# Performance work log

Hardware: AMD Instinct MI355X
Metric: run time of the kernel (lower is better)

Reference implementation:

```python
import jax, jax.numpy as jnp
import numpy as np

HEADS = 8
D = 1024


def setup_inputs() -> dict:
    key = jax.random.key(0)
    ks = jax.random.split(key, 10)
    B, Sq, Sk = 8, 2048, 2048
    x = jax.random.normal(ks[0], (B, Sq, D), dtype=jnp.float32)
    context = jax.random.normal(ks[1], (B, Sk, D), dtype=jnp.float32)
    # Dense params (glorot-ish scale)
    def dense(k, fin, fout):
        return jax.random.normal(k, (fin, fout), dtype=jnp.float32) / np.sqrt(fin)
    Wq = dense(ks[2], D, HEADS); bq = jnp.zeros((HEADS,), jnp.float32)
    Wk = dense(ks[3], D, HEADS); bk = jnp.zeros((HEADS,), jnp.float32)
    Wv = dense(ks[4], D, HEADS); bv = jnp.zeros((HEADS,), jnp.float32)
    Wo = dense(ks[5], HEADS, D); bo = jnp.zeros((D,), jnp.float32)
    return {"x": x, "context": context, "Wq": Wq, "bq": bq,
            "Wk": Wk, "bk": bk, "Wv": Wv, "bv": bv, "Wo": Wo, "bo": bo}


def reference(x, context, Wq, bq, Wk, bk, Wv, bv, Wo, bo):
    # q: [B,Sq,H], k/v: [B,Sk,H]  (H = heads = projection width, no head split)
    q = jnp.einsum('bsd,dh->bsh', x, Wq) + bq
    k = jnp.einsum('btd,dh->bth', context, Wk) + bk
    v = jnp.einsum('btd,dh->bth', context, Wv) + bv
    # Dot(axes=-1): scores[b,s,t] = q[b,s,:] . k[b,t,:]  -> [B,Sq,Sk]
    scores = jnp.einsum('bsh,bth->bst', q, k)
    weights = jax.nn.softmax(scores, axis=-1)  # no 1/sqrt(d) scaling in original
    # Dot(axes=(-1,1)): out[b,s,h] = sum_t weights[b,s,t] * v[b,t,h]
    out = jnp.einsum('bst,bth->bsh', weights, v)
    return jnp.einsum('bsh,hd->bsd', out, Wo) + bo
```

## Files before the change

### kernel.cpp

```cpp
#include <hip/hip_runtime.h>

constexpr int D = 1024;
constexpr int H = 8;
constexpr int S = 2048;
constexpr int B = 8;
constexpr int NROW = B * S;

__global__ __launch_bounds__(512)
void proj_kernel(const float* __restrict__ x, const float* __restrict__ ctx,
                 const float* __restrict__ Wq, const float* __restrict__ bq,
                 const float* __restrict__ Wk, const float* __restrict__ bk,
                 const float* __restrict__ Wv, const float* __restrict__ bv,
                 float* __restrict__ qo, float* __restrict__ ko,
                 float* __restrict__ vo)
{
    __shared__ float part[8][64][17];
    const int tid  = threadIdx.x;
    const int lane = tid & 63;
    const int wid  = __builtin_amdgcn_readfirstlane(tid >> 6);
    const bool kv  = (int)blockIdx.x >= (NROW / 64);
    const int blk  = kv ? ((int)blockIdx.x - NROW / 64) : (int)blockIdx.x;
    const int row  = blk * 64 + lane;

    const float4* s4 = (const float4*)((kv ? ctx : x) + (size_t)row * D);
    const int kf0 = wid * 32;

    float acc[16];
#pragma unroll
    for (int c = 0; c < 16; ++c) acc[c] = 0.f;

    if (!kv) {
#pragma unroll 4
        for (int j = 0; j < 32; ++j) {
            const float4 xr = s4[kf0 + j];
            const int k0 = (kf0 + j) * 4;
#pragma unroll
            for (int e = 0; e < 4; ++e) {
                const float xs = (&xr.x)[e];
                const float* wr = Wq + (size_t)(k0 + e) * 8;
#pragma unroll
                for (int h = 0; h < 8; ++h) acc[h] += xs * wr[h];
            }
        }
    } else {
#pragma unroll 2
        for (int j = 0; j < 32; ++j) {
            const float4 xr = s4[kf0 + j];
            const int k0 = (kf0 + j) * 4;
#pragma unroll
            for (int e = 0; e < 4; ++e) {
                const float xs = (&xr.x)[e];
                const float* wkr = Wk + (size_t)(k0 + e) * 8;
                const float* wvr = Wv + (size_t)(k0 + e) * 8;
#pragma unroll
                for (int h = 0; h < 8; ++h) {
                    acc[h]     += xs * wkr[h];
                    acc[8 + h] += xs * wvr[h];
                }
            }
        }
    }

#pragma unroll
    for (int c = 0; c < 16; ++c) part[wid][lane][c] = acc[c];
    __syncthreads();

    const int r = tid >> 3, h = tid & 7;
    const int orow = blk * 64 + r;
    if (!kv) {
        float s0 = 0.f;
#pragma unroll
        for (int w = 0; w < 8; ++w) s0 += part[w][r][h];
        qo[(size_t)orow * H + h] = s0 + bq[h];
    } else {
        float s0 = 0.f, s1 = 0.f;
#pragma unroll
        for (int w = 0; w < 8; ++w) { s0 += part[w][r][h]; s1 += part[w][r][h + 8]; }
        ko[(size_t)orow * H + h] = s0 + bk[h];
        vo[(size_t)orow * H + h] = s1 + bv[h];
    }
}

constexpr int ROWS_PER_WAVE = 4;
constexpr int ROWS_PER_BLOCK = 16;
constexpr int TILE_T = 512;

__global__ __launch_bounds__(256)
void attn_kernel(const float* __restrict__ q, const float* __restrict__ k,
                 const float* __restrict__ v, const float* __restrict__ Wo,
                 const float* __restrict__ bo, float* __restrict__ out)
{
    __shared__ float4 kt[TILE_T * 2];
    __shared__ float4 vt[TILE_T * 2];
    const int tid  = threadIdx.x;
    const int lane = tid & 63;
    const int wid  = tid >> 6;

    const int row0 = blockIdx.x * ROWS_PER_BLOCK + wid * ROWS_PER_WAVE;
    const int b = row0 >> 11;

    float qv[ROWS_PER_WAVE][H];
#pragma unroll
    for (int r = 0; r < ROWS_PER_WAVE; ++r) {
        const float4* q4 = (const float4*)(q + (size_t)(row0 + r) * H);
        const float4 a = q4[0], c = q4[1];
        qv[r][0] = a.x; qv[r][1] = a.y; qv[r][2] = a.z; qv[r][3] = a.w;
        qv[r][4] = c.x; qv[r][5] = c.y; qv[r][6] = c.z; qv[r][7] = c.w;
    }

    float l[ROWS_PER_WAVE] = {0.f, 0.f, 0.f, 0.f};
    float o[ROWS_PER_WAVE][H];
#pragma unroll
    for (int r = 0; r < ROWS_PER_WAVE; ++r)
#pragma unroll
        for (int h = 0; h < H; ++h) o[r][h] = 0.f;

    const float4* kg = (const float4*)(k + (size_t)b * S * H);
    const float4* vg = (const float4*)(v + (size_t)b * S * H);

    for (int tile = 0; tile < S / TILE_T; ++tile) {
        __syncthreads();
#pragma unroll
        for (int i = 0; i < 4; ++i) {
            kt[i * 256 + tid] = kg[tile * 1024 + i * 256 + tid];
            vt[i * 256 + tid] = vg[tile * 1024 + i * 256 + tid];
        }
        __syncthreads();
#pragma unroll 2
        for (int m = 0; m < TILE_T / 64; ++m) {
            const int t2 = (lane + (m << 6)) * 2;
            const float4 ka = kt[t2], kb = kt[t2 + 1];
            const float4 va = vt[t2], vb = vt[t2 + 1];
#pragma unroll
            for (int r = 0; r < ROWS_PER_WAVE; ++r) {
                const float s = qv[r][0] * ka.x + qv[r][1] * ka.y
                              + qv[r][2] * ka.z + qv[r][3] * ka.w
                              + qv[r][4] * kb.x + qv[r][5] * kb.y
                              + qv[r][6] * kb.z + qv[r][7] * kb.w;
                const float e = __expf(s);
                l[r] += e;
                o[r][0] += e * va.x; o[r][1] += e * va.y;
                o[r][2] += e * va.z; o[r][3] += e * va.w;
                o[r][4] += e * vb.x; o[r][5] += e * vb.y;
                o[r][6] += e * vb.z; o[r][7] += e * vb.w;
            }
        }
    }

#pragma unroll
    for (int r = 0; r < ROWS_PER_WAVE; ++r) {
#pragma unroll
        for (int off = 32; off > 0; off >>= 1) l[r] += __shfl_xor(l[r], off);
        const float inv = 1.f / l[r];
#pragma unroll
        for (int h = 0; h < H; ++h) {
#pragma unroll
            for (int off = 32; off > 0; off >>= 1) o[r][h] += __shfl_xor(o[r][h], off);
            o[r][h] *= inv;
        }
    }

    const float4* Wo4 = (const float4*)Wo;
    const float4* bo4 = (const float4*)bo;
    float4* out4 = (float4*)out;
#pragma unroll
    for (int c = 0; c < 4; ++c) {
        const int f = lane + 64 * c;
        float4 w[H];
#pragma unroll
        for (int h = 0; h < H; ++h) w[h] = Wo4[h * (D / 4) + f];
        const float4 base = bo4[f];
#pragma unroll
        for (int r = 0; r < ROWS_PER_WAVE; ++r) {
            float4 acc = base;
#pragma unroll
            for (int h = 0; h < H; ++h) {
                acc.x += o[r][h] * w[h].x;
                acc.y += o[r][h] * w[h].y;
                acc.z += o[r][h] * w[h].z;
                acc.w += o[r][h] * w[h].w;
            }
            out4[(size_t)(row0 + r) * (D / 4) + f] = acc;
        }
    }
}

extern "C" void kernel_launch(void* const* d_in, const int* in_sizes, int n_in,
                              void* d_out, int out_size, void* d_ws, size_t ws_size,
                              hipStream_t stream) {
    const float* x   = (const float*)d_in[0];
    const float* ctx = (const float*)d_in[1];
    const float* Wq  = (const float*)d_in[2];
    const float* bq  = (const float*)d_in[3];
    const float* Wk  = (const float*)d_in[4];
    const float* bk  = (const float*)d_in[5];
    const float* Wv  = (const float*)d_in[6];
    const float* bv  = (const float*)d_in[7];
    const float* Wo  = (const float*)d_in[8];
    const float* bo  = (const float*)d_in[9];
    float* out = (float*)d_out;

    float* qw = (float*)d_ws;
    float* kw = qw + (size_t)NROW * H;
    float* vw = kw + (size_t)NROW * H;

    proj_kernel<<<dim3(2 * NROW / 64), dim3(512), 0, stream>>>(
        x, ctx, Wq, bq, Wk, bk, Wv, bv, qw, kw, vw);
    attn_kernel<<<dim3(NROW / ROWS_PER_BLOCK), dim3(256), 0, stream>>>(
        qw, kw, vw, Wo, bo, out);
}
```

Before: 236.7 us.

## Stage projection weights in swizzled LDS and use 16-lane teams per row pair

The projection kernel now copies Wq (or Wk and Wv) into shared memory with an XOR swizzle, instead of reading the weights from global memory or scalar loads inside the inner loop. Each 16-thread team handles two rows, with lanes striding across the feature dimension so global loads are coalesced. Partial sums are reduced with shuffles rather than through a shared-memory partial array and a second sync. The cost is a larger LDS footprint (64KB for K/V blocks), which may reduce occupancy, plus per-block weight staging overhead.

```diff
diff --git a/kernel.cpp b/kernel.cpp
--- a/kernel.cpp
+++ b/kernel.cpp
@@ -5,6 +5,8 @@
 constexpr int S = 2048;
 constexpr int B = 8;
 constexpr int NROW = B * S;
+
+__device__ __forceinline__ int swz(int i) { return i ^ ((i >> 3) & 7); }
 
 __global__ __launch_bounds__(512)
 void proj_kernel(const float* __restrict__ x, const float* __restrict__ ctx,
@@ -14,70 +16,105 @@
                  float* __restrict__ qo, float* __restrict__ ko,
                  float* __restrict__ vo)
 {
-    __shared__ float part[8][64][17];
-    const int tid  = threadIdx.x;
-    const int lane = tid & 63;
-    const int wid  = __builtin_amdgcn_readfirstlane(tid >> 6);
-    const bool kv  = (int)blockIdx.x >= (NROW / 64);
-    const int blk  = kv ? ((int)blockIdx.x - NROW / 64) : (int)blockIdx.x;
-    const int row  = blk * 64 + lane;
-
-    const float4* s4 = (const float4*)((kv ? ctx : x) + (size_t)row * D);
-    const int kf0 = wid * 32;
-
-    float acc[16];
-#pragma unroll
-    for (int c = 0; c < 16; ++c) acc[c] = 0.f;
-
-    if (!kv) {
+    __shared__ float4 wlds[4096];
+    const int tid = threadIdx.x;
+    const bool kvb = (int)blockIdx.x >= (NROW / 64);
+    const int blk  = kvb ? ((int)blockIdx.x - NROW / 64) : (int)blockIdx.x;
+
+    if (!kvb) {
+        const float4* w4 = (const float4*)Wq;
+        for (int i = tid; i < 2048; i += 512) wlds[swz(i)] = w4[i];
+    } else {
+        const float4* a4 = (const float4*)Wk;
+        const float4* b4 = (const float4*)Wv;
+        for (int i = tid; i < 2048; i += 512) {
+            wlds[swz(i)]        = a4[i];
+            wlds[2048 + swz(i)] = b4[i];
+        }
+    }
+    __syncthreads();
+
+    const int c    = tid & 15;
+    const int team = tid >> 4;
+    const int row0 = blk * 64 + team * 2;
+    const float* src = kvb ? ctx : x;
+    const float4* r0 = (const float4*)(src + (size_t)row0 * D);
+    const float4* r1 = (const float4*)(src + (size_t)(row0 + 1) * D);
+
+    if (!kvb) {
+        float a0[8], a1[8];
+#pragma unroll
+        for (int h = 0; h < 8; ++h) { a0[h] = 0.f; a1[h] = 0.f; }
 #pragma unroll 4
-        for (int j = 0; j < 32; ++j) {
-            const float4 xr = s4[kf0 + j];
-            const int k0 = (kf0 + j) * 4;
+        for (int j = 0; j < 16; ++j) {
+            const float4 xa = r0[16 * j + c];
+            const float4 xb = r1[16 * j + c];
+            const int ib = 128 * j + 8 * c;
 #pragma unroll
             for (int e = 0; e < 4; ++e) {
-                const float xs = (&xr.x)[e];
-                const float* wr = Wq + (size_t)(k0 + e) * 8;
-#pragma unroll
-                for (int h = 0; h < 8; ++h) acc[h] += xs * wr[h];
+                const float4 w0 = wlds[swz(ib + 2 * e)];
+                const float4 w1 = wlds[swz(ib + 2 * e + 1)];
+                const float s0 = (&xa.x)[e], s1 = (&xb.x)[e];
+                a0[0] += s0 * w0.x; a0[1] += s0 * w0.y; a0[2] += s0 * w0.z; a0[3] += s0 * w0.w;
+                a0[4] += s0 * w1.x; a0[5] += s0 * w1.y; a0[6] += s0 * w1.z; a0[7] += s0 * w1.w;
+                a1[0] += s1 * w0.x; a1[1] += s1 * w0.y; a1[2] += s1 * w0.z; a1[3] += s1 * w0.w;
+                a1[4] += s1 * w1.x; a1[5] += s1 * w1.y; a1[6] += s1 * w1.z; a1[7] += s1 * w1.w;
+            }
+        }
+#pragma unroll
+        for (int h = 0; h < 8; ++h) {
+            float s0 = a0[h], s1 = a1[h];
+            s0 += __shfl_down(s0, 8); s1 += __shfl_down(s1, 8);
+            s0 += __shfl_down(s0, 4); s1 += __shfl_down(s1, 4);
+            s0 += __shfl_down(s0, 2); s1 += __shfl_down(s1, 2);
+            s0 += __shfl_down(s0, 1); s1 += __shfl_down(s1, 1);
+            if (c == 0) {
+                qo[(size_t)row0 * H + h]       = s0 + bq[h];
+                qo[(size_t)(row0 + 1) * H + h] = s1 + bq[h];
             }
         }
     } else {
+        float a0[16], a1[16];
+#pragma unroll
+        for (int h = 0; h < 16; ++h) { a0[h] = 0.f; a1[h] = 0.f; }
 #pragma unroll 2
-        for (int j = 0; j < 32; ++j) {
-            const float4 xr = s4[kf0 + j];
-            const int k0 = (kf0 + j) * 4;
+        for (int j = 0; j < 16; ++j) {
+            const float4 xa = r0[16 * j + c];
+            const float4 xb = r1[16 * j + c];
+            const int ib = 128 * j + 8 * c;
 #pragma unroll
             for (int e = 0; e < 4; ++e) {
-                const float xs = (&xr.x)[e];
-                const float* wkr = Wk + (size_t)(k0 + e) * 8;
-                const float* wvr = Wv + (size_t)(k0 + e) * 8;
-#pragma unroll
-                for (int h = 0; h < 8; ++h) {
-                    acc[h]     += xs * wkr[h];
-                    acc[8 + h] += xs * wvr[h];
+                const int i0 = swz(ib + 2 * e), i1 = swz(ib + 2 * e + 1);
+                const float4 k0 = wlds[i0],        k1 = wlds[i1];
+                const float4 v0 = wlds[2048 + i0], v1 = wlds[2048 + i1];
+                const float s0 = (&xa.x)[e], s1 = (&xb.x)[e];
+                a0[0]  += s0 * k0.x; a0[1]  += s0 * k0.y; a0[2]  += s0 * k0.z; a0[3]  += s0 * k0.w;
+                a0[4]  += s0 * k1.x; a0[5]  += s0 * k1.y; a0[6]  += s0 * k1.z; a0[7]  += s0 * k1.w;
+                a0[8]  += s0 * v0.x; a0[9]  += s0 * v0.y; a0[10] += s0 * v0.z; a0[11] += s0 * v0.w;
+                a0[12] += s0 * v1.x; a0[13] += s0 * v1.y; a0[14] += s0 * v1.z; a0[15] += s0 * v1.w;
+                a1[0]  += s1 * k0.x; a1[1]  += s1 * k0.y; a1[2]  += s1 * k0.z; a1[3]  += s1 * k0.w;
+                a1[4]  += s1 * k1.x; a1[5]  += s1 * k1.y; a1[6]  += s1 * k1.z; a1[7]  += s1 * k1.w;
+                a1[8]  += s1 * v0.x; a1[9]  += s1 * v0.y; a1[10] += s1 * v0.z; a1[11] += s1 * v0.w;
+                a1[12] += s1 * v1.x; a1[13] += s1 * v1.y; a1[14] += s1 * v1.z; a1[15] += s1 * v1.w;
+            }
+        }
+#pragma unroll
+        for (int h = 0; h < 16; ++h) {
+            float s0 = a0[h], s1 = a1[h];
+            s0 += __shfl_down(s0, 8); s1 += __shfl_down(s1, 8);
+            s0 += __shfl_down(s0, 4); s1 += __shfl_down(s1, 4);
+            s0 += __shfl_down(s0, 2); s1 += __shfl_down(s1, 2);
+            s0 += __shfl_down(s0, 1); s1 += __shfl_down(s1, 1);
+            if (c == 0) {
+                if (h < 8) {
+                    ko[(size_t)row0 * H + h]       = s0 + bk[h];
+                    ko[(size_t)(row0 + 1) * H + h] = s1 + bk[h];
+                } else {
+                    vo[(size_t)row0 * H + (h - 8)]       = s0 + bv[h - 8];
+                    vo[(size_t)(row0 + 1) * H + (h - 8)] = s1 + bv[h - 8];
                 }
             }
         }
-    }
-
-#pragma unroll
-    for (int c = 0; c < 16; ++c) part[wid][lane][c] = acc[c];
-    __syncthreads();
-
-    const int r = tid >> 3, h = tid & 7;
-    const int orow = blk * 64 + r;
-    if (!kv) {
-        float s0 = 0.f;
-#pragma unroll
-        for (int w = 0; w < 8; ++w) s0 += part[w][r][h];
-        qo[(size_t)orow * H + h] = s0 + bq[h];
-    } else {
-        float s0 = 0.f, s1 = 0.f;
-#pragma unroll
-        for (int w = 0; w < 8; ++w) { s0 += part[w][r][h]; s1 += part[w][r][h + 8]; }
-        ko[(size_t)orow * H + h] = s0 + bk[h];
-        vo[(size_t)orow * H + h] = s1 + bv[h];
     }
 }
 
```

New measurement: 230.9 us. 1.03x faster.

## Stage projection weights in LDS and split K/V projections into separate blocks

Applied to the files above, without the earlier changes.

The projection kernel now loads the full 1024x8 weight matrix for its projection into shared memory, then computes one projection per block using 256 threads with four K-slices per row. K and V get separate blocks instead of one fused block, giving more, lighter blocks with 8 accumulators each. Weight reads come from LDS rather than per-lane global loads, and register pressure drops. The trade-off is that the context tensor is now read twice from global memory, once for K and once for V, and each block must first copy the weights into LDS.

```diff
diff --git a/kernel.cpp b/kernel.cpp
--- a/kernel.cpp
+++ b/kernel.cpp
@@ -6,7 +6,7 @@
 constexpr int B = 8;
 constexpr int NROW = B * S;
 
-__global__ __launch_bounds__(512)
+__global__ __launch_bounds__(256)
 void proj_kernel(const float* __restrict__ x, const float* __restrict__ ctx,
                  const float* __restrict__ Wq, const float* __restrict__ bq,
                  const float* __restrict__ Wk, const float* __restrict__ bk,
@@ -14,70 +14,59 @@
                  float* __restrict__ qo, float* __restrict__ ko,
                  float* __restrict__ vo)
 {
-    __shared__ float part[8][64][17];
-    const int tid  = threadIdx.x;
-    const int lane = tid & 63;
-    const int wid  = __builtin_amdgcn_readfirstlane(tid >> 6);
-    const bool kv  = (int)blockIdx.x >= (NROW / 64);
-    const int blk  = kv ? ((int)blockIdx.x - NROW / 64) : (int)blockIdx.x;
-    const int row  = blk * 64 + lane;
-
-    const float4* s4 = (const float4*)((kv ? ctx : x) + (size_t)row * D);
-    const int kf0 = wid * 32;
-
-    float acc[16];
-#pragma unroll
-    for (int c = 0; c < 16; ++c) acc[c] = 0.f;
-
-    if (!kv) {
-#pragma unroll 4
-        for (int j = 0; j < 32; ++j) {
-            const float4 xr = s4[kf0 + j];
-            const int k0 = (kf0 + j) * 4;
-#pragma unroll
-            for (int e = 0; e < 4; ++e) {
-                const float xs = (&xr.x)[e];
-                const float* wr = Wq + (size_t)(k0 + e) * 8;
-#pragma unroll
-                for (int h = 0; h < 8; ++h) acc[h] += xs * wr[h];
-            }
-        }
-    } else {
-#pragma unroll 2
-        for (int j = 0; j < 32; ++j) {
-            const float4 xr = s4[kf0 + j];
-            const int k0 = (kf0 + j) * 4;
-#pragma unroll
-            for (int e = 0; e < 4; ++e) {
-                const float xs = (&xr.x)[e];
-                const float* wkr = Wk + (size_t)(k0 + e) * 8;
-                const float* wvr = Wv + (size_t)(k0 + e) * 8;
-#pragma unroll
-                for (int h = 0; h < 8; ++h) {
-                    acc[h]     += xs * wkr[h];
-                    acc[8 + h] += xs * wvr[h];
-                }
-            }
-        }
-    }
-
-#pragma unroll
-    for (int c = 0; c < 16; ++c) part[wid][lane][c] = acc[c];
+    __shared__ float4 wlds[2048];
+    __shared__ float  part[4 * 64 * 9];
+
+    const int bid = blockIdx.x;
+    int type, blk;
+    if (bid < NROW / 64) { type = 0; blk = bid; }
+    else { const int sub = bid - NROW / 64; blk = sub >> 1; type = 1 + (sub & 1); }
+
+    const float* W   = (type == 0) ? Wq : (type == 1) ? Wk : Wv;
+    const float* bb  = (type == 0) ? bq : (type == 1) ? bk : bv;
+    const float* src = (type == 0) ? x  : ctx;
+    float* dst       = (type == 0) ? qo : (type == 1) ? ko : vo;
+
+    const int tid = threadIdx.x, lane = tid & 63, w = tid >> 6;
+
+    const float4* W4 = (const float4*)W;
+    for (int i = tid; i < 2048; i += 256) wlds[i] = W4[i];
     __syncthreads();
 
-    const int r = tid >> 3, h = tid & 7;
-    const int orow = blk * 64 + r;
-    if (!kv) {
-        float s0 = 0.f;
-#pragma unroll
-        for (int w = 0; w < 8; ++w) s0 += part[w][r][h];
-        qo[(size_t)orow * H + h] = s0 + bq[h];
-    } else {
-        float s0 = 0.f, s1 = 0.f;
-#pragma unroll
-        for (int w = 0; w < 8; ++w) { s0 += part[w][r][h]; s1 += part[w][r][h + 8]; }
-        ko[(size_t)orow * H + h] = s0 + bk[h];
-        vo[(size_t)orow * H + h] = s1 + bv[h];
+    const int row = blk * 64 + lane;
+    const float4* r4 = (const float4*)(src + (size_t)row * D) + (w << 6);
+
+    float acc[8];
+#pragma unroll
+    for (int h = 0; h < 8; ++h) acc[h] = 0.f;
+
+#pragma unroll 8
+    for (int j = 0; j < 64; ++j) {
+        const float4 xv = r4[j];
+        const int kb = (w << 9) + (j << 3);
+#pragma unroll
+        for (int e = 0; e < 4; ++e) {
+            const float4 w0 = wlds[kb + 2 * e];
+            const float4 w1 = wlds[kb + 2 * e + 1];
+            const float xs = (&xv.x)[e];
+            acc[0] += xs * w0.x; acc[1] += xs * w0.y;
+            acc[2] += xs * w0.z; acc[3] += xs * w0.w;
+            acc[4] += xs * w1.x; acc[5] += xs * w1.y;
+            acc[6] += xs * w1.z; acc[7] += xs * w1.w;
+        }
+    }
+
+    const int pb = tid * 9;
+#pragma unroll
+    for (int h = 0; h < 8; ++h) part[pb + h] = acc[h];
+    __syncthreads();
+
+#pragma unroll
+    for (int idx = tid; idx < 512; idx += 256) {
+        const int r = idx >> 3, h = idx & 7;
+        const float s = part[r * 9 + h] + part[(64 + r) * 9 + h]
+                      + part[(128 + r) * 9 + h] + part[(192 + r) * 9 + h];
+        dst[(size_t)(blk * 64 + r) * H + h] = s + bb[h];
     }
 }
 
@@ -204,7 +193,7 @@
     float* kw = qw + (size_t)NROW * H;
     float* vw = kw + (size_t)NROW * H;
 
-    proj_kernel<<<dim3(2 * NROW / 64), dim3(512), 0, stream>>>(
+    proj_kernel<<<dim3(3 * NROW / 64), dim3(256), 0, stream>>>(
         x, ctx, Wq, bq, Wk, bk, Wv, bv, qw, kw, vw);
     attn_kernel<<<dim3(NROW / ROWS_PER_BLOCK), dim3(256), 0, stream>>>(
         qw, kw, vw, Wo, bo, out);
```

Result: slower. 251.4 us (+6.2%).
